# Kernel optimization log

Hardware: AMD Instinct MI355X
Metric: run time of the kernel (lower is better)

## Reference

```python
import jax, jax.numpy as jnp
import numpy as np

N_NODES = 100000
N_EDGES = 1250000
IN_NDIM = 128
OUT_NDIM = 64


def setup_inputs() -> dict:
    key = jax.random.key(0)
    ks = jax.random.split(key, 8)
    return {
        "node_feats": jax.random.normal(ks[0], (N_NODES, IN_NDIM), dtype=jnp.float32),
        "edge_d": jax.random.uniform(ks[1], (N_EDGES, 1), dtype=jnp.float32),
        "W0": jax.random.normal(ks[2], (1, 1), dtype=jnp.float32),
        "W1": jax.random.normal(ks[3], (OUT_NDIM, IN_NDIM), dtype=jnp.float32) * (IN_NDIM ** -0.5),
        "W2": jax.random.normal(ks[4], (OUT_NDIM, IN_NDIM), dtype=jnp.float32) * (IN_NDIM ** -0.5),
        "Wa": jax.random.normal(ks[5], (1, 2 * OUT_NDIM + 1), dtype=jnp.float32) * (OUT_NDIM ** -0.5),
        "src": jax.random.randint(ks[6], (N_EDGES,), 0, N_NODES, dtype=jnp.int32),
        "dst": jax.random.randint(ks[7], (N_EDGES,), 0, N_NODES, dtype=jnp.int32),
    }


def reference(node_feats, edge_d, W0, W1, W2, Wa, src, dst):
    N = node_feats.shape[0]
    # fc1 / fc2 node projections (bias-free linears)
    z = node_feats @ W1.T            # [N, out_ndim]
    z_i = node_feats @ W2.T          # [N, out_ndim]
    # fc0 edge feature projection
    t = edge_d @ W0.T                # [E, 1]
    # gather per-edge endpoint features
    z_src = z[src]                   # [E, out_ndim]
    z_dst = z[dst]                   # [E, out_ndim]
    # attention logit: leaky_relu(attn_fc([z_src, z_dst, t]))
    a = jnp.concatenate([z_src, z_dst, t], axis=1) @ Wa.T   # [E, 1]
    e = jax.nn.leaky_relu(a[:, 0], 0.01)                      # torch default slope
    # segment softmax over incoming edges of each dst node
    m = jax.ops.segment_max(e, dst, num_segments=N)          # -inf for empty segs
    ex = jnp.exp(e - m[dst])
    denom = jax.ops.segment_sum(ex, dst, num_segments=N)
    alpha = ex / denom[dst]                                   # [E]
    # weighted scatter-sum of source messages
    z_neighbor = jax.ops.segment_sum(alpha[:, None] * z_src, dst, num_segments=N)
    h = jax.nn.relu(z_i + z_neighbor)
    return h
```

## Files before the change

### kernel.cpp

```cpp
#include <hip/hip_runtime.h>

#define N_NODES 100000
#define N_EDGES 1250000
#define IN_D 128
#define OUT_D 64
#define BSHIFT 8
#define NBUCK  391
#define CAP    4608
#define EPB    8192
#define NBLK_E ((N_EDGES + EPB - 1) / EPB)
#define NBLK_G 1563

typedef __attribute__((ext_vector_type(8))) __bf16 bf16x8;
typedef __attribute__((ext_vector_type(4))) float floatx4;

__device__ __forceinline__ float2 up2(unsigned u) {
    return make_float2(__uint_as_float(u << 16),
                       __uint_as_float(u & 0xFFFF0000u));
}

__global__ __launch_bounds__(256) void fusedA_kernel(
    const float* __restrict__ x, const float* __restrict__ W1,
    const float* __restrict__ W2, const float* __restrict__ Wa,
    const int* __restrict__ dst, const int* __restrict__ src,
    const float* __restrict__ edge_d,
    int* __restrict__ gcur, uint2* __restrict__ payA,
    unsigned short* __restrict__ zb, unsigned short* __restrict__ zib,
    float* __restrict__ s1, float* __restrict__ s2)
{
    __shared__ __bf16 sB[16384];
    __shared__ float  sWa[128];
    __shared__ int    h[NBUCK];
    __shared__ int    lcur[NBUCK];

    const int t = threadIdx.x;

    if (blockIdx.x < NBLK_E) {
        for (int i = t; i < NBUCK; i += 256) h[i] = 0;
        __syncthreads();
        const int base = blockIdx.x * EPB;
        for (int k0 = 0; k0 < EPB; k0 += 1024) {
            int i = base + k0 + t * 4;
            if (i < N_EDGES) {
                int4 d4 = *(const int4*)(dst + i);
                atomicAdd(&h[d4.x >> BSHIFT], 1);
                atomicAdd(&h[d4.y >> BSHIFT], 1);
                atomicAdd(&h[d4.z >> BSHIFT], 1);
                atomicAdd(&h[d4.w >> BSHIFT], 1);
            }
        }
        __syncthreads();
        for (int b = t; b < NBUCK; b += 256) {
            int hc = h[b];
            int p = hc ? atomicAdd(&gcur[b], hc) : 0;
            lcur[b] = b * CAP + p;
        }
        __syncthreads();
        #define EMIT(dv, sv, ev)                                              \
            { int bk = (dv) >> BSHIFT;                                        \
              int pos = atomicAdd(&lcur[bk], 1);                              \
              if (pos < (bk + 1) * CAP)                                       \
                  payA[pos] = make_uint2((unsigned)(sv) |                     \
                                         ((unsigned)((dv) & 255) << 17),      \
                                         __float_as_uint(ev)); }
        for (int k0 = 0; k0 < EPB; k0 += 1024) {
            int i = base + k0 + t * 4;
            if (i < N_EDGES) {
                int4   d4 = *(const int4*)(dst + i);
                int4   s4 = *(const int4*)(src + i);
                float4 e4 = *(const float4*)(edge_d + i);
                EMIT(d4.x, s4.x, e4.x);
                EMIT(d4.y, s4.y, e4.y);
                EMIT(d4.z, s4.z, e4.z);
                EMIT(d4.w, s4.w, e4.w);
            }
        }
        #undef EMIT
        return;
    }

    for (int i = t; i < 16384; i += 256) {
        int j    = i & 7;
        int lane = (i >> 3) & 63;
        int blk  = i >> 9;
        int nt = blk >> 2, kc = blk & 3;
        int n = nt * 16 + (lane & 15);
        int k = kc * 32 + (lane >> 4) * 8 + j;
        float w = (n < 64) ? W1[n * 128 + k] : W2[(n - 64) * 128 + k];
        sB[i] = (__bf16)w;
    }
    if (t < 128) sWa[t] = Wa[t];
    __syncthreads();

    const int lane = t & 63;
    const int wave = t >> 6;
    const int tile = (blockIdx.x - NBLK_E) * 4 + wave;
    if (tile * 16 >= N_NODES) return;

    const int n0 = tile * 16;
    const int m  = lane & 15;
    const int kb = lane >> 4;

    floatx4 acc[8];
    #pragma unroll
    for (int q = 0; q < 8; ++q) acc[q] = (floatx4)(0.f);

    const float* xrow = x + (size_t)(n0 + m) * IN_D;

    #pragma unroll
    for (int kc = 0; kc < 4; ++kc) {
        float4 v0 = *(const float4*)(xrow + kc * 32 + kb * 8);
        float4 v1 = *(const float4*)(xrow + kc * 32 + kb * 8 + 4);
        float xs[8] = {v0.x, v0.y, v0.z, v0.w, v1.x, v1.y, v1.z, v1.w};
        bf16x8 ahi, alo;
        #pragma unroll
        for (int j = 0; j < 8; ++j) {
            __bf16 hh = (__bf16)xs[j];
            ahi[j] = hh;
            alo[j] = (__bf16)(xs[j] - (float)hh);
        }
        #pragma unroll
        for (int nt = 0; nt < 8; ++nt) {
            int off = ((nt * 4 + kc) * 64 + lane) * 8;
            bf16x8 b = *(const bf16x8*)(sB + off);
            acc[nt] = __builtin_amdgcn_mfma_f32_16x16x32_bf16(ahi, b, acc[nt], 0, 0, 0);
            acc[nt] = __builtin_amdgcn_mfma_f32_16x16x32_bf16(alo, b, acc[nt], 0, 0, 0);
        }
    }

    #pragma unroll
    for (int nt = 0; nt < 8; ++nt) {
        int col = (nt & 3) * 16 + m;
        unsigned short* dp = (nt < 4) ? zb : zib;
        #pragma unroll
        for (int reg = 0; reg < 4; ++reg) {
            int row = n0 + kb * 4 + reg;
            __bf16 hh = (__bf16)acc[nt][reg];
            dp[(size_t)row * OUT_D + col] = *(unsigned short*)&hh;
        }
    }

    #pragma unroll
    for (int reg = 0; reg < 4; ++reg) {
        float p1 = 0.f, p2 = 0.f;
        #pragma unroll
        for (int nt = 0; nt < 4; ++nt) {
            float zv = acc[nt][reg];
            p1 += zv * sWa[nt * 16 + m];
            p2 += zv * sWa[64 + nt * 16 + m];
        }
        #pragma unroll
        for (int off = 8; off > 0; off >>= 1) {
            p1 += __shfl_xor(p1, off);
            p2 += __shfl_xor(p2, off);
        }
        if (m == 0) {
            int row = n0 + kb * 4 + reg;
            s1[row] = p1;
            s2[row] = p2;
        }
    }
}

__global__ __launch_bounds__(256) void passB_kernel(
    const int* __restrict__ gcur, const float* __restrict__ s1,
    const float* __restrict__ s2, const float* __restrict__ W0,
    const float* __restrict__ Wa, const uint2* __restrict__ payA,
    int2* __restrict__ node_meta, uint2* __restrict__ payB)
{
    __shared__ int   h[256];
    __shared__ int   lc[256];
    __shared__ int   sm[256];
    __shared__ float s2s[256];

    const int b = blockIdx.x, t = threadIdx.x;
    const int base = b * CAP;
    const int cnt = min(gcur[b], CAP);
    const int n0 = b << BSHIFT;
    const float tc = W0[0] * Wa[2 * OUT_D];

    h[t] = 0;
    s2s[t] = (n0 + t < N_NODES) ? s2[n0 + t] : 0.f;
    __syncthreads();

    for (int i0 = t * 2; i0 < cnt; i0 += 512) {
        uint4 u = *(const uint4*)(payA + base + i0);
        atomicAdd(&h[(u.x >> 17) & 255], 1);
        if (i0 + 1 < cnt) atomicAdd(&h[(u.z >> 17) & 255], 1);
    }
    __syncthreads();

    int v = h[t];
    sm[t] = v;
    __syncthreads();
    for (int off = 1; off < 256; off <<= 1) {
        int add = (t >= off) ? sm[t - off] : 0;
        __syncthreads();
        sm[t] += add;
        __syncthreads();
    }
    int start = base + sm[t] - v;
    lc[t] = start;
    if (n0 + t < N_NODES) node_meta[n0 + t] = make_int2(start, v);
    __syncthreads();

    for (int i0 = t * 2; i0 < cnt; i0 += 512) {
        uint4 u = *(const uint4*)(payA + base + i0);
        bool v2 = (i0 + 1 < cnt);
        int sj0 = u.x & 0x1FFFF;
        int sj1 = u.z & 0x1FFFF;
        float s1a = s1[sj0];
        float s1b = v2 ? s1[sj1] : 0.f;

        int j0 = (u.x >> 17) & 255;
        float a0 = fmaf(tc, __uint_as_float(u.y), s1a + s2s[j0]);
        float e0 = (a0 > 0.f) ? a0 : 0.01f * a0;
        int p0 = atomicAdd(&lc[j0], 1);
        payB[p0] = make_uint2((unsigned)sj0, __float_as_uint(__expf(e0)));

        if (v2) {
            int j1 = (u.z >> 17) & 255;
            float a1 = fmaf(tc, __uint_as_float(u.w), s1b + s2s[j1]);
            float e1 = (a1 > 0.f) ? a1 : 0.01f * a1;
            int p1 = atomicAdd(&lc[j1], 1);
            payB[p1] = make_uint2((unsigned)sj1, __float_as_uint(__expf(e1)));
        }
    }
}

__global__ __launch_bounds__(256) void gather_finalize_kernel(
    const int2* __restrict__ node_meta, const uint2* __restrict__ payB,
    const unsigned short* __restrict__ zb, const unsigned short* __restrict__ zib,
    float* __restrict__ out)
{
    __shared__ uint2 buf[8][32];

    const int lane = threadIdx.x & 63;
    const int wave = threadIdx.x >> 6;
    const int half = lane >> 5;
    const int lh   = lane & 31;
    const int nodeSlot = wave * 2 + half;
    const int d = blockIdx.x * 8 + nodeSlot;

    const int2 meta = node_meta[d];
    const int beg = meta.x;
    const int len = meta.y;

    const int eC = lh >> 3;
    const int c  = lh & 7;

    float den = 0.f;
    float2 a0 = make_float2(0.f, 0.f), a1 = a0, a2 = a0, a3 = a0;

    for (int o = 0; o < len; o += 32) {
        int rem = len - o;
        bool v = lh < rem;
        uint2 p = payB[beg + o + (v ? lh : 0)];
        den += v ? __uint_as_float(p.y) : 0.f;
        if (v) buf[nodeSlot][lh] = p;

        int cnt = min(32, rem);
        for (int g = 0; g * 4 < cnt; ++g) {
            int j = g * 4 + eC;
            uint2 pe = buf[nodeSlot][(j < cnt) ? j : 0];
            float exe = (j < cnt) ? __uint_as_float(pe.y) : 0.f;
            uint4 zv = *(const uint4*)(zb + (size_t)pe.x * OUT_D + c * 8);
            float2 w0 = up2(zv.x), w1 = up2(zv.y), w2 = up2(zv.z), w3 = up2(zv.w);
            a0.x = fmaf(exe, w0.x, a0.x); a0.y = fmaf(exe, w0.y, a0.y);
            a1.x = fmaf(exe, w1.x, a1.x); a1.y = fmaf(exe, w1.y, a1.y);
            a2.x = fmaf(exe, w2.x, a2.x); a2.y = fmaf(exe, w2.y, a2.y);
            a3.x = fmaf(exe, w3.x, a3.x); a3.y = fmaf(exe, w3.y, a3.y);
        }
    }

    #pragma unroll
    for (int off = 16; off > 0; off >>= 1) den += __shfl_xor(den, off);
    #pragma unroll
    for (int off = 8; off <= 16; off <<= 1) {
        a0.x += __shfl_xor(a0.x, off); a0.y += __shfl_xor(a0.y, off);
        a1.x += __shfl_xor(a1.x, off); a1.y += __shfl_xor(a1.y, off);
        a2.x += __shfl_xor(a2.x, off); a2.y += __shfl_xor(a2.y, off);
        a3.x += __shfl_xor(a3.x, off); a3.y += __shfl_xor(a3.y, off);
    }

    if (lh < 8) {
        float inv = (den > 0.f) ? 1.f / den : 0.f;
        uint4 zv = *(const uint4*)(zib + (size_t)d * OUT_D + lh * 8);
        float2 w0 = up2(zv.x), w1 = up2(zv.y), w2 = up2(zv.z), w3 = up2(zv.w);
        float4 o0, o1;
        o0.x = fmaxf(w0.x + a0.x * inv, 0.f);
        o0.y = fmaxf(w0.y + a0.y * inv, 0.f);
        o0.z = fmaxf(w1.x + a1.x * inv, 0.f);
        o0.w = fmaxf(w1.y + a1.y * inv, 0.f);
        o1.x = fmaxf(w2.x + a2.x * inv, 0.f);
        o1.y = fmaxf(w2.y + a2.y * inv, 0.f);
        o1.z = fmaxf(w3.x + a3.x * inv, 0.f);
        o1.w = fmaxf(w3.y + a3.y * inv, 0.f);
        *(float4*)(out + (size_t)d * OUT_D + lh * 8)     = o0;
        *(float4*)(out + (size_t)d * OUT_D + lh * 8 + 4) = o1;
    }
}

extern "C" void kernel_launch(void* const* d_in, const int* in_sizes, int n_in,
                              void* d_out, int out_size, void* d_ws, size_t ws_size,
                              hipStream_t stream) {
    const float* node_feats = (const float*)d_in[0];
    const float* edge_d     = (const float*)d_in[1];
    const float* W0         = (const float*)d_in[2];
    const float* W1         = (const float*)d_in[3];
    const float* W2         = (const float*)d_in[4];
    const float* Wa         = (const float*)d_in[5];
    const int*   src        = (const int*)d_in[6];
    const int*   dst        = (const int*)d_in[7];
    float* out = (float*)d_out;

    char* ws = (char*)d_ws;
    uint2* payA = (uint2*)ws;    ws += (size_t)NBUCK * CAP * 8;
    uint2* payB = (uint2*)ws;    ws += (size_t)NBUCK * CAP * 8;
    unsigned short* zbuf = (unsigned short*)ws; ws += (size_t)N_NODES * OUT_D * 2;
    unsigned short* zib  = (unsigned short*)ws; ws += (size_t)N_NODES * OUT_D * 2;
    float* s1 = (float*)ws;      ws += (size_t)N_NODES * 4;
    float* s2 = (float*)ws;      ws += (size_t)N_NODES * 4;
    int2*  node_meta = (int2*)ws; ws += (size_t)N_NODES * 8;
    int*   gcur = (int*)ws;      ws += ((NBUCK + 3) & ~3) * 4;

    hipMemsetAsync(gcur, 0, NBUCK * 4, stream);

    fusedA_kernel<<<NBLK_E + NBLK_G, 256, 0, stream>>>(
        node_feats, W1, W2, Wa, dst, src, edge_d,
        gcur, payA, zbuf, zib, s1, s2);

    passB_kernel<<<NBUCK, 256, 0, stream>>>(
        gcur, s1, s2, W0, Wa, payA, node_meta, payB);

    gather_finalize_kernel<<<N_NODES / 8, 256, 0, stream>>>(
        node_meta, payB, zbuf, zib, out);
}
```

Before: 198.8 us.

## Move attention logit and exp into gather kernel, slim bucket pass

The per-edge leaky-relu logit and exp move out of the bucket-sort pass (passB) and into the gather/finalize kernel. passB becomes a pure index permutation: it now runs 512 threads per block, and each thread handles 4 edges. The constant W0*Wa[128] is folded into the edge payload during pass A, and the edge partition block size is halved. The W1/W2 staging into shared memory is vectorized with float4 loads and 16-byte bf16x8 stores. The gather kernel now does random s1 loads per edge, and passB's prefix scan relies on matched barrier counts across divergent branches.

Result: faster. 191.2 us (-3.8%).

```diff
diff --git a/kernel.cpp b/kernel.cpp
--- a/kernel.cpp
+++ b/kernel.cpp
@@ -7,8 +7,8 @@
 #define BSHIFT 8
 #define NBUCK  391
 #define CAP    4608
-#define EPB    8192
-#define NBLK_E ((N_EDGES + EPB - 1) / EPB)
+#define EPB    4096
+#define NBLK_E 306
 #define NBLK_G 1563
 
 typedef __attribute__((ext_vector_type(8))) __bf16 bf16x8;
@@ -21,7 +21,8 @@
 
 __global__ __launch_bounds__(256) void fusedA_kernel(
     const float* __restrict__ x, const float* __restrict__ W1,
-    const float* __restrict__ W2, const float* __restrict__ Wa,
+    const float* __restrict__ W2, const float* __restrict__ W0,
+    const float* __restrict__ Wa,
     const int* __restrict__ dst, const int* __restrict__ src,
     const float* __restrict__ edge_d,
     int* __restrict__ gcur, uint2* __restrict__ payA,
@@ -36,6 +37,7 @@
     const int t = threadIdx.x;
 
     if (blockIdx.x < NBLK_E) {
+        const float tc = W0[0] * Wa[2 * OUT_D];
         for (int i = t; i < NBUCK; i += 256) h[i] = 0;
         __syncthreads();
         const int base = blockIdx.x * EPB;
@@ -62,7 +64,7 @@
               if (pos < (bk + 1) * CAP)                                       \
                   payA[pos] = make_uint2((unsigned)(sv) |                     \
                                          ((unsigned)((dv) & 255) << 17),      \
-                                         __float_as_uint(ev)); }
+                                         __float_as_uint(tc * (ev))); }
         for (int k0 = 0; k0 < EPB; k0 += 1024) {
             int i = base + k0 + t * 4;
             if (i < N_EDGES) {
@@ -79,15 +81,22 @@
         return;
     }
 
-    for (int i = t; i < 16384; i += 256) {
-        int j    = i & 7;
-        int lane = (i >> 3) & 63;
-        int blk  = i >> 9;
-        int nt = blk >> 2, kc = blk & 3;
-        int n = nt * 16 + (lane & 15);
-        int k = kc * 32 + (lane >> 4) * 8 + j;
-        float w = (n < 64) ? W1[n * 128 + k] : W2[(n - 64) * 128 + k];
-        sB[i] = (__bf16)w;
+    #pragma unroll
+    for (int g = 0; g < 8; ++g) {
+        int gi = t + g * 256;
+        int n  = gi >> 4;
+        int k8 = gi & 15;
+        const float* wrow = (n < 64) ? (W1 + n * 128) : (W2 + (n - 64) * 128);
+        float4 v0 = *(const float4*)(wrow + k8 * 8);
+        float4 v1 = *(const float4*)(wrow + k8 * 8 + 4);
+        int lane = ((k8 & 3) << 4) | (n & 15);
+        int off  = (((n >> 4) * 4 + (k8 >> 2)) * 64 + lane) * 8;
+        bf16x8 bb;
+        bb[0] = (__bf16)v0.x; bb[1] = (__bf16)v0.y;
+        bb[2] = (__bf16)v0.z; bb[3] = (__bf16)v0.w;
+        bb[4] = (__bf16)v1.x; bb[5] = (__bf16)v1.y;
+        bb[6] = (__bf16)v1.z; bb[7] = (__bf16)v1.w;
+        *(bf16x8*)(sB + off) = bb;
     }
     if (t < 128) sWa[t] = Wa[t];
     __syncthreads();
@@ -162,74 +171,71 @@
     }
 }
 
-__global__ __launch_bounds__(256) void passB_kernel(
-    const int* __restrict__ gcur, const float* __restrict__ s1,
-    const float* __restrict__ s2, const float* __restrict__ W0,
-    const float* __restrict__ Wa, const uint2* __restrict__ payA,
+__global__ __launch_bounds__(512) void passB_kernel(
+    const int* __restrict__ gcur, const uint2* __restrict__ payA,
     int2* __restrict__ node_meta, uint2* __restrict__ payB)
 {
-    __shared__ int   h[256];
-    __shared__ int   lc[256];
-    __shared__ int   sm[256];
-    __shared__ float s2s[256];
+    __shared__ int h[256];
+    __shared__ int lc[256];
+    __shared__ int sm[256];
 
     const int b = blockIdx.x, t = threadIdx.x;
     const int base = b * CAP;
     const int cnt = min(gcur[b], CAP);
     const int n0 = b << BSHIFT;
-    const float tc = W0[0] * Wa[2 * OUT_D];
-
-    h[t] = 0;
-    s2s[t] = (n0 + t < N_NODES) ? s2[n0 + t] : 0.f;
+
+    if (t < 256) h[t] = 0;
     __syncthreads();
 
-    for (int i0 = t * 2; i0 < cnt; i0 += 512) {
-        uint4 u = *(const uint4*)(payA + base + i0);
-        atomicAdd(&h[(u.x >> 17) & 255], 1);
-        if (i0 + 1 < cnt) atomicAdd(&h[(u.z >> 17) & 255], 1);
+    for (int i0 = t * 4; i0 < cnt; i0 += 2048) {
+        uint4 u0 = *(const uint4*)(payA + base + i0);
+        uint4 u1 = *(const uint4*)(payA + base + i0 + 2);
+        atomicAdd(&h[(u0.x >> 17) & 255], 1);
+        if (i0 + 1 < cnt) atomicAdd(&h[(u0.z >> 17) & 255], 1);
+        if (i0 + 2 < cnt) atomicAdd(&h[(u1.x >> 17) & 255], 1);
+        if (i0 + 3 < cnt) atomicAdd(&h[(u1.z >> 17) & 255], 1);
     }
     __syncthreads();
 
-    int v = h[t];
-    sm[t] = v;
+    if (t < 256) {
+        int v = h[t];
+        sm[t] = v;
+        __syncthreads();
+        for (int off = 1; off < 256; off <<= 1) {
+            int add = (t >= off) ? sm[t - off] : 0;
+            __syncthreads();
+            sm[t] += add;
+            __syncthreads();
+        }
+        int start = base + sm[t] - v;
+        lc[t] = start;
+        if (n0 + t < N_NODES) node_meta[n0 + t] = make_int2(start, v);
+    } else {
+        __syncthreads();
+        for (int off = 1; off < 256; off <<= 1) {
+            __syncthreads(); __syncthreads();
+        }
+    }
     __syncthreads();
-    for (int off = 1; off < 256; off <<= 1) {
-        int add = (t >= off) ? sm[t - off] : 0;
-        __syncthreads();
-        sm[t] += add;
-        __syncthreads();
-    }
-    int start = base + sm[t] - v;
-    lc[t] = start;
-    if (n0 + t < N_NODES) node_meta[n0 + t] = make_int2(start, v);
-    __syncthreads();
-
-    for (int i0 = t * 2; i0 < cnt; i0 += 512) {
-        uint4 u = *(const uint4*)(payA + base + i0);
-        bool v2 = (i0 + 1 < cnt);
-        int sj0 = u.x & 0x1FFFF;
-        int sj1 = u.z & 0x1FFFF;
-        float s1a = s1[sj0];
-        float s1b = v2 ? s1[sj1] : 0.f;
-
-        int j0 = (u.x >> 17) & 255;
-        float a0 = fmaf(tc, __uint_as_float(u.y), s1a + s2s[j0]);
-        float e0 = (a0 > 0.f) ? a0 : 0.01f * a0;
-        int p0 = atomicAdd(&lc[j0], 1);
-        payB[p0] = make_uint2((unsigned)sj0, __float_as_uint(__expf(e0)));
-
-        if (v2) {
-            int j1 = (u.z >> 17) & 255;
-            float a1 = fmaf(tc, __uint_as_float(u.w), s1b + s2s[j1]);
-            float e1 = (a1 > 0.f) ? a1 : 0.01f * a1;
-            int p1 = atomicAdd(&lc[j1], 1);
-            payB[p1] = make_uint2((unsigned)sj1, __float_as_uint(__expf(e1)));
-        }
-    }
+
+    #define PUT(xx, yy, ok)                                                   \
+        if (ok) { int j = ((xx) >> 17) & 255;                                 \
+                  int pos = atomicAdd(&lc[j], 1);                             \
+                  payB[pos] = make_uint2((xx) & 0x1FFFFu, (yy)); }
+    for (int i0 = t * 4; i0 < cnt; i0 += 2048) {
+        uint4 u0 = *(const uint4*)(payA + base + i0);
+        uint4 u1 = *(const uint4*)(payA + base + i0 + 2);
+        PUT(u0.x, u0.y, true);
+        PUT(u0.z, u0.w, i0 + 1 < cnt);
+        PUT(u1.x, u1.y, i0 + 2 < cnt);
+        PUT(u1.z, u1.w, i0 + 3 < cnt);
+    }
+    #undef PUT
 }
 
 __global__ __launch_bounds__(256) void gather_finalize_kernel(
     const int2* __restrict__ node_meta, const uint2* __restrict__ payB,
+    const float* __restrict__ s1, const float* __restrict__ s2,
     const unsigned short* __restrict__ zb, const unsigned short* __restrict__ zib,
     float* __restrict__ out)
 {
@@ -245,6 +251,7 @@
     const int2 meta = node_meta[d];
     const int beg = meta.x;
     const int len = meta.y;
+    const float s2d = s2[d];
 
     const int eC = lh >> 3;
     const int c  = lh & 7;
@@ -256,8 +263,14 @@
         int rem = len - o;
         bool v = lh < rem;
         uint2 p = payB[beg + o + (v ? lh : 0)];
-        den += v ? __uint_as_float(p.y) : 0.f;
-        if (v) buf[nodeSlot][lh] = p;
+        float ex = 0.f;
+        if (v) {
+            float a = __uint_as_float(p.y) + s1[p.x] + s2d;
+            float e = (a > 0.f) ? a : 0.01f * a;
+            ex = __expf(e);
+            buf[nodeSlot][lh] = make_uint2(p.x, __float_as_uint(ex));
+        }
+        den += ex;
 
         int cnt = min(32, rem);
         for (int g = 0; g * 4 < cnt; ++g) {
@@ -327,12 +340,11 @@
     hipMemsetAsync(gcur, 0, NBUCK * 4, stream);
 
     fusedA_kernel<<<NBLK_E + NBLK_G, 256, 0, stream>>>(
-        node_feats, W1, W2, Wa, dst, src, edge_d,
+        node_feats, W1, W2, W0, Wa, dst, src, edge_d,
         gcur, payA, zbuf, zib, s1, s2);
 
-    passB_kernel<<<NBUCK, 256, 0, stream>>>(
-        gcur, s1, s2, W0, Wa, payA, node_meta, payB);
+    passB_kernel<<<NBUCK, 512, 0, stream>>>(gcur, payA, node_meta, payB);
 
     gather_finalize_kernel<<<N_NODES / 8, 256, 0, stream>>>(
-        node_meta, payB, zbuf, zib, out);
-}
+        node_meta, payB, s1, s2, zbuf, zib, out);
+}
```
